# Kernel tuning notes

Measured on AMD Instinct MI355X. Metric: run time of the kernel, lower is better.

The kernel has to match this reference:

```python
import jax, jax.numpy as jnp
import numpy as np

N_NODES = 100000
N_EDGES = 3200000

def setup_inputs() -> dict:
    key = jax.random.key(0)
    ks = jax.random.split(key, 6)
    x = jax.random.normal(ks[0], (N_NODES, 128), dtype=jnp.float32)
    edge_index = jax.random.randint(ks[1], (2, N_EDGES), 0, N_NODES, dtype=jnp.int64)
    W1 = jax.random.normal(ks[2], (128, 64), dtype=jnp.float32) * 0.05
    b1 = jnp.zeros((64,), dtype=jnp.float32)
    W2 = jax.random.normal(ks[3], (64, 64), dtype=jnp.float32) * 0.05
    b2 = jnp.zeros((64,), dtype=jnp.float32)
    Wf = jax.random.normal(ks[4], (64, 40), dtype=jnp.float32) * 0.05
    bf = jnp.zeros((40,), dtype=jnp.float32)
    return {"x": x, "edge_index": edge_index, "W1": W1, "b1": b1,
            "W2": W2, "b2": b2, "Wf": Wf, "bf": bf}

def _gcn_graph(edge_index, n_nodes):
    # Add self loops (PyG GCNConv default), compute symmetric norm.
    loop = jnp.arange(n_nodes, dtype=edge_index.dtype)
    src = jnp.concatenate([edge_index[0], loop])
    dst = jnp.concatenate([edge_index[1], loop])
    deg = jax.ops.segment_sum(jnp.ones_like(dst, dtype=jnp.float32), dst,
                              num_segments=n_nodes)
    dinv = jnp.where(deg > 0, jax.lax.rsqrt(deg), 0.0)
    norm = dinv[src] * dinv[dst]  # [E+N]
    return src, dst, norm

def _gcn_layer(x, W, b, src, dst, norm, n_nodes):
    h = x @ W                     # transform first (as PyG GCNConv)
    msg = h[src] * norm[:, None]  # gather + scale
    agg = jax.ops.segment_sum(msg, dst, num_segments=n_nodes)  # scatter-sum
    return agg + b

def reference(x, edge_index, W1, b1, W2, b2, Wf, bf):
    n = x.shape[0]
    src, dst, norm = _gcn_graph(edge_index, n)
    h = jax.nn.relu(_gcn_layer(x, W1, b1, src, dst, norm, n))
    h = jax.nn.relu(_gcn_layer(h, W2, b2, src, dst, norm, n))
    logits = h @ Wf + bf
    return jax.nn.log_softmax(logits, axis=1)
```

## Files before the change

### kernel.cpp

```cpp
#include <hip/hip_runtime.h>
#include <hip/hip_fp16.h>
#include <cstdint>
#include <cstddef>
#include <cmath>


#define T1  4096
#define CAP 12288

typedef _Float16 half8 __attribute__((ext_vector_type(8)));
typedef float f32x4 __attribute__((ext_vector_type(4)));
typedef float f32x2 __attribute__((ext_vector_type(2)));

__global__ __launch_bounds__(512) void k_init(int* __restrict__ cursor1, int NB) {
    int t = threadIdx.x;
    for (int i = t; i < NB; i += 512) cursor1[i] = i * CAP;
}

__global__ __launch_bounds__(256) void k_pass1(const int* __restrict__ src,
        const int* __restrict__ dst, int* __restrict__ cursor1,
        unsigned int* __restrict__ tmp, int E, int NB) {
    __shared__ unsigned int pack[T1];
    __shared__ unsigned short bkt[T1];
    __shared__ int h[512], hs_[512], gbase[512];
    int t = threadIdx.x;
    for (int i = t; i < 512; i += 256) h[i] = 0;
    __syncthreads();
    int base = blockIdx.x * T1;
    int n = min(T1, E - base);
    unsigned int pk[16];
    int bl[16];
    #pragma unroll
    for (int i = 0; i < 16; ++i) {
        int idx = i * 256 + t;
        if (idx < n) {
            int s_ = src[base + idx], d = dst[base + idx];
            int b = d >> 8;
            pk[i] = (unsigned int)s_ | ((unsigned int)(d & 255) << 17);
            int lo = atomicAdd(&h[b], 1);
            bl[i] = (b << 13) | lo;
        } else bl[i] = -1;
    }
    __syncthreads();
    hs_[t] = h[t]; hs_[t + 256] = h[t + 256];
    __syncthreads();
    for (int st = 1; st < 512; st <<= 1) {
        int v0 = (t >= st) ? hs_[t - st] : 0;
        int v1 = (t + 256 >= st) ? hs_[t + 256 - st] : 0;
        __syncthreads();
        hs_[t] += v0; hs_[t + 256] += v1;
        __syncthreads();
    }
    for (int i = t; i < NB; i += 256)
        gbase[i] = h[i] ? atomicAdd(&cursor1[i], h[i]) : 0;
    __syncthreads();
    #pragma unroll
    for (int i = 0; i < 16; ++i) {
        if (bl[i] >= 0) {
            int b = bl[i] >> 13, lo = bl[i] & 8191;
            int slot = hs_[b] - h[b] + lo;
            pack[slot] = pk[i];
            bkt[slot]  = (unsigned short)b;
        }
    }
    __syncthreads();
    for (int s_ = t; s_ < n; s_ += 256) {
        int b = bkt[s_];
        tmp[gbase[b] + (s_ - (hs_[b] - h[b]))] = pack[s_];
    }
}

__global__ __launch_bounds__(256) void k_p2(const unsigned int* __restrict__ tmp,
        const int* __restrict__ cursor1, int* __restrict__ rowptr,
        int* __restrict__ cnt, int* __restrict__ csrc,
        float* __restrict__ dinv, int N) {
    __shared__ int c[256], cur[256];
    int t = threadIdx.x, b = blockIdx.x;
    c[t] = 0;
    __syncthreads();
    int s0 = b * CAP, s1 = cursor1[b];
    for (int s = s0 + t; s < s1; s += 256)
        atomicAdd(&c[(tmp[s] >> 17) & 255], 1);
    __syncthreads();
    int v = c[t];
    cur[t] = v;
    __syncthreads();
    for (int st = 1; st < 256; st <<= 1) {
        int p = (t >= st) ? cur[t - st] : 0;
        __syncthreads();
        cur[t] += p;
        __syncthreads();
    }
    int rp = s0 + cur[t] - v;
    int node = b * 256 + t;
    if (node < N) {
        rowptr[node] = rp;
        cnt[node]    = v;
        dinv[node]   = rsqrtf((float)v + 1.0f);
    }
    cur[t] = rp;
    __syncthreads();
    for (int s = s0 + t; s < s1; s += 256) {
        unsigned int p = tmp[s];
        int q = atomicAdd(&cur[(p >> 17) & 255], 1);
        csrc[q] = (int)(p & 0x1FFFFu);
    }
}

__global__ __launch_bounds__(256) void k_agg(const int* __restrict__ rowptr,
        const int* __restrict__ cnt, const int* __restrict__ csrc,
        const unsigned int* __restrict__ hp, float* __restrict__ acc, int N) {
    int w = (blockIdx.x * 256 + threadIdx.x) >> 6;
    int lane = threadIdx.x & 63;
    if (w >= N) return;
    int grp = lane >> 4, sub = lane & 15;
    int rs = rowptr[w], re = rs + cnt[w];
    float a0 = 0.f, a1 = 0.f, a2 = 0.f, a3 = 0.f;
    if (grp == 0) {
        unsigned v = hp[((size_t)w << 4) + sub];
        f32x2 lo = __builtin_amdgcn_cvt_pk_f32_fp8((int)v, false);
        f32x2 hi = __builtin_amdgcn_cvt_pk_f32_fp8((int)v, true);
        a0 = lo[0]; a1 = lo[1]; a2 = hi[0]; a3 = hi[1];
    }
    int e = rs + grp;
    for (; e + 12 < re; e += 16) {
        int u0 = csrc[e], u1 = csrc[e + 4], u2 = csrc[e + 8], u3 = csrc[e + 12];
        unsigned v0 = hp[((size_t)u0 << 4) + sub];
        unsigned v1 = hp[((size_t)u1 << 4) + sub];
        unsigned v2 = hp[((size_t)u2 << 4) + sub];
        unsigned v3 = hp[((size_t)u3 << 4) + sub];
        f32x2 l0 = __builtin_amdgcn_cvt_pk_f32_fp8((int)v0, false);
        f32x2 h0 = __builtin_amdgcn_cvt_pk_f32_fp8((int)v0, true);
        f32x2 l1 = __builtin_amdgcn_cvt_pk_f32_fp8((int)v1, false);
        f32x2 h1 = __builtin_amdgcn_cvt_pk_f32_fp8((int)v1, true);
        f32x2 l2 = __builtin_amdgcn_cvt_pk_f32_fp8((int)v2, false);
        f32x2 h2 = __builtin_amdgcn_cvt_pk_f32_fp8((int)v2, true);
        f32x2 l3 = __builtin_amdgcn_cvt_pk_f32_fp8((int)v3, false);
        f32x2 h3 = __builtin_amdgcn_cvt_pk_f32_fp8((int)v3, true);
        a0 += l0[0]; a1 += l0[1]; a2 += h0[0]; a3 += h0[1];
        a0 += l1[0]; a1 += l1[1]; a2 += h1[0]; a3 += h1[1];
        a0 += l2[0]; a1 += l2[1]; a2 += h2[0]; a3 += h2[1];
        a0 += l3[0]; a1 += l3[1]; a2 += h3[0]; a3 += h3[1];
    }
    for (; e < re; e += 4) {
        unsigned v = hp[((size_t)csrc[e] << 4) + sub];
        f32x2 lo = __builtin_amdgcn_cvt_pk_f32_fp8((int)v, false);
        f32x2 hi = __builtin_amdgcn_cvt_pk_f32_fp8((int)v, true);
        a0 += lo[0]; a1 += lo[1]; a2 += hi[0]; a3 += hi[1];
    }
    a0 += __shfl_xor(a0, 16, 64); a0 += __shfl_xor(a0, 32, 64);
    a1 += __shfl_xor(a1, 16, 64); a1 += __shfl_xor(a1, 32, 64);
    a2 += __shfl_xor(a2, 16, 64); a2 += __shfl_xor(a2, 32, 64);
    a3 += __shfl_xor(a3, 16, 64); a3 += __shfl_xor(a3, 32, 64);
    if (grp == 0) {
        float* op = acc + ((size_t)w << 6) + sub;
        op[0]  = a0;
        op[16] = a1;
        op[32] = a2;
        op[48] = a3;
    }
}

__global__ __launch_bounds__(256) void k_xform1(const float* __restrict__ x,
        const float* __restrict__ W1, const float* __restrict__ dinv,
        unsigned int* __restrict__ hs, int N, int ntiles) {
    int t = threadIdx.x;
    int lane = t & 63, wid = t >> 6;
    int r16 = lane & 15, kg = lane >> 4;
    half8 bf[4][4];
    #pragma unroll
    for (int ct = 0; ct < 4; ++ct)
        #pragma unroll
        for (int kt = 0; kt < 4; ++kt) {
            const float* wp = W1 + (kt * 32 + kg * 8) * 64 + ct * 16 + r16;
            half8 h;
            #pragma unroll
            for (int j = 0; j < 8; ++j) h[j] = (_Float16)wp[j * 64];
            bf[ct][kt] = h;
        }
    int wtile = blockIdx.x * 4 + wid;
    int nw = gridDim.x * 4;
    for (int tile = wtile; tile < ntiles; tile += nw) {
        int v0 = tile * 16;
        int rowA = min(v0 + r16, N - 1);
        const float* xp = x + (size_t)rowA * 128 + kg * 8;
        half8 af[4];
        #pragma unroll
        for (int kt = 0; kt < 4; ++kt) {
            float4 p = *(const float4*)(xp + kt * 32);
            float4 q = *(const float4*)(xp + kt * 32 + 4);
            half8 a;
            a[0] = (_Float16)p.x; a[1] = (_Float16)p.y;
            a[2] = (_Float16)p.z; a[3] = (_Float16)p.w;
            a[4] = (_Float16)q.x; a[5] = (_Float16)q.y;
            a[6] = (_Float16)q.z; a[7] = (_Float16)q.w;
            af[kt] = a;
        }
        f32x4 acc0 = {0,0,0,0}, acc1 = {0,0,0,0}, acc2 = {0,0,0,0}, acc3 = {0,0,0,0};
        #pragma unroll
        for (int kt = 0; kt < 4; ++kt) {
            acc0 = __builtin_amdgcn_mfma_f32_16x16x32_f16(af[kt], bf[0][kt], acc0, 0, 0, 0);
            acc1 = __builtin_amdgcn_mfma_f32_16x16x32_f16(af[kt], bf[1][kt], acc1, 0, 0, 0);
            acc2 = __builtin_amdgcn_mfma_f32_16x16x32_f16(af[kt], bf[2][kt], acc2, 0, 0, 0);
            acc3 = __builtin_amdgcn_mfma_f32_16x16x32_f16(af[kt], bf[3][kt], acc3, 0, 0, 0);
        }
        #pragma unroll
        for (int r = 0; r < 4; ++r) {
            int node = v0 + kg * 4 + r;
            if (node < N) {
                float d = dinv[node];
                int pk = __builtin_amdgcn_cvt_pk_fp8_f32(d * acc0[r], d * acc1[r], 0, false);
                pk     = __builtin_amdgcn_cvt_pk_fp8_f32(d * acc2[r], d * acc3[r], pk, true);
                hs[((size_t)node << 4) + r16] = (unsigned int)pk;
            }
        }
    }
}

__global__ __launch_bounds__(256) void k_xform2(const float* __restrict__ acc_in,
        const float* __restrict__ W2, const float* __restrict__ b1,
        const float* __restrict__ dinv, unsigned int* __restrict__ hs2, int N, int ntiles) {
    int t = threadIdx.x;
    int lane = t & 63, wid = t >> 6;
    int r16 = lane & 15, kg = lane >> 4;
    half8 bf[4][2];
    #pragma unroll
    for (int ct = 0; ct < 4; ++ct)
        #pragma unroll
        for (int kt = 0; kt < 2; ++kt) {
            const float* wp = W2 + (kt * 32 + kg * 8) * 64 + ct * 16 + r16;
            half8 h;
            #pragma unroll
            for (int j = 0; j < 8; ++j) h[j] = (_Float16)wp[j * 64];
            bf[ct][kt] = h;
        }
    float b1r[2][8];
    #pragma unroll
    for (int kt = 0; kt < 2; ++kt)
        #pragma unroll
        for (int j = 0; j < 8; ++j) b1r[kt][j] = b1[kt * 32 + kg * 8 + j];
    int wtile = blockIdx.x * 4 + wid;
    int nw = gridDim.x * 4;
    for (int tile = wtile; tile < ntiles; tile += nw) {
        int v0 = tile * 16;
        int rowA = min(v0 + r16, N - 1);
        float da = dinv[rowA];
        const float* ap = acc_in + ((size_t)rowA << 6) + kg * 8;
        half8 af[2];
        #pragma unroll
        for (int kt = 0; kt < 2; ++kt) {
            float4 p = *(const float4*)(ap + kt * 32);
            float4 q = *(const float4*)(ap + kt * 32 + 4);
            half8 a;
            a[0] = (_Float16)fmaxf(fmaf(da, p.x, b1r[kt][0]), 0.f);
            a[1] = (_Float16)fmaxf(fmaf(da, p.y, b1r[kt][1]), 0.f);
            a[2] = (_Float16)fmaxf(fmaf(da, p.z, b1r[kt][2]), 0.f);
            a[3] = (_Float16)fmaxf(fmaf(da, p.w, b1r[kt][3]), 0.f);
            a[4] = (_Float16)fmaxf(fmaf(da, q.x, b1r[kt][4]), 0.f);
            a[5] = (_Float16)fmaxf(fmaf(da, q.y, b1r[kt][5]), 0.f);
            a[6] = (_Float16)fmaxf(fmaf(da, q.z, b1r[kt][6]), 0.f);
            a[7] = (_Float16)fmaxf(fmaf(da, q.w, b1r[kt][7]), 0.f);
            af[kt] = a;
        }
        f32x4 acc0 = {0,0,0,0}, acc1 = {0,0,0,0}, acc2 = {0,0,0,0}, acc3 = {0,0,0,0};
        #pragma unroll
        for (int kt = 0; kt < 2; ++kt) {
            acc0 = __builtin_amdgcn_mfma_f32_16x16x32_f16(af[kt], bf[0][kt], acc0, 0, 0, 0);
            acc1 = __builtin_amdgcn_mfma_f32_16x16x32_f16(af[kt], bf[1][kt], acc1, 0, 0, 0);
            acc2 = __builtin_amdgcn_mfma_f32_16x16x32_f16(af[kt], bf[2][kt], acc2, 0, 0, 0);
            acc3 = __builtin_amdgcn_mfma_f32_16x16x32_f16(af[kt], bf[3][kt], acc3, 0, 0, 0);
        }
        #pragma unroll
        for (int r = 0; r < 4; ++r) {
            int node = v0 + kg * 4 + r;
            if (node < N) {
                float d = dinv[node];
                int pk = __builtin_amdgcn_cvt_pk_fp8_f32(d * acc0[r], d * acc1[r], 0, false);
                pk     = __builtin_amdgcn_cvt_pk_fp8_f32(d * acc2[r], d * acc3[r], pk, true);
                hs2[((size_t)node << 4) + r16] = (unsigned int)pk;
            }
        }
    }
}

__global__ __launch_bounds__(256) void k_final(const float* __restrict__ acc2,
        const float* __restrict__ Wf, const float* __restrict__ b2,
        const float* __restrict__ bf, const float* __restrict__ dinv,
        float* __restrict__ out, int N, int ntiles) {
    int t = threadIdx.x;
    int lane = t & 63, wid = t >> 6;
    int r16 = lane & 15, kg = lane >> 4;
    half8 bfr[3][2];
    #pragma unroll
    for (int ct = 0; ct < 3; ++ct)
        #pragma unroll
        for (int kt = 0; kt < 2; ++kt) {
            int col = ct * 16 + r16;
            half8 h;
            #pragma unroll
            for (int j = 0; j < 8; ++j) {
                int k = kt * 32 + kg * 8 + j;
                h[j] = (col < 40) ? (_Float16)Wf[k * 40 + col] : (_Float16)0.f;
            }
            bfr[ct][kt] = h;
        }
    float b2r[2][8];
    #pragma unroll
    for (int kt = 0; kt < 2; ++kt)
        #pragma unroll
        for (int j = 0; j < 8; ++j) b2r[kt][j] = b2[kt * 32 + kg * 8 + j];
    float bf0 = bf[r16];
    float bf1 = bf[16 + r16];
    float bf2 = (r16 < 8) ? bf[32 + r16] : 0.f;
    int wtile = blockIdx.x * 4 + wid;
    int nw = gridDim.x * 4;
    for (int tile = wtile; tile < ntiles; tile += nw) {
        int v0 = tile * 16;
        int rowA = min(v0 + r16, N - 1);
        float da = dinv[rowA];
        const float* ap = acc2 + ((size_t)rowA << 6) + kg * 8;
        half8 af[2];
        #pragma unroll
        for (int kt = 0; kt < 2; ++kt) {
            float4 p = *(const float4*)(ap + kt * 32);
            float4 q = *(const float4*)(ap + kt * 32 + 4);
            half8 a;
            a[0] = (_Float16)fmaxf(fmaf(da, p.x, b2r[kt][0]), 0.f);
            a[1] = (_Float16)fmaxf(fmaf(da, p.y, b2r[kt][1]), 0.f);
            a[2] = (_Float16)fmaxf(fmaf(da, p.z, b2r[kt][2]), 0.f);
            a[3] = (_Float16)fmaxf(fmaf(da, p.w, b2r[kt][3]), 0.f);
            a[4] = (_Float16)fmaxf(fmaf(da, q.x, b2r[kt][4]), 0.f);
            a[5] = (_Float16)fmaxf(fmaf(da, q.y, b2r[kt][5]), 0.f);
            a[6] = (_Float16)fmaxf(fmaf(da, q.z, b2r[kt][6]), 0.f);
            a[7] = (_Float16)fmaxf(fmaf(da, q.w, b2r[kt][7]), 0.f);
            af[kt] = a;
        }
        f32x4 a0 = {0,0,0,0}, a1 = {0,0,0,0}, a2 = {0,0,0,0};
        #pragma unroll
        for (int kt = 0; kt < 2; ++kt) {
            a0 = __builtin_amdgcn_mfma_f32_16x16x32_f16(af[kt], bfr[0][kt], a0, 0, 0, 0);
            a1 = __builtin_amdgcn_mfma_f32_16x16x32_f16(af[kt], bfr[1][kt], a1, 0, 0, 0);
            a2 = __builtin_amdgcn_mfma_f32_16x16x32_f16(af[kt], bfr[2][kt], a2, 0, 0, 0);
        }
        #pragma unroll
        for (int r = 0; r < 4; ++r) {
            float z0 = a0[r] + bf0;
            float z1 = a1[r] + bf1;
            float z2 = (r16 < 8) ? (a2[r] + bf2) : -INFINITY;
            float m = fmaxf(fmaxf(z0, z1), z2);
            #pragma unroll
            for (int o = 8; o; o >>= 1) m = fmaxf(m, __shfl_xor(m, o, 64));
            float s = expf(z0 - m) + expf(z1 - m) + ((r16 < 8) ? expf(z2 - m) : 0.f);
            #pragma unroll
            for (int o = 8; o; o >>= 1) s += __shfl_xor(s, o, 64);
            float ls = m + logf(s);
            int node = v0 + kg * 4 + r;
            if (node < N) {
                float* op = out + (size_t)node * 40;
                op[r16]      = z0 - ls;
                op[16 + r16] = z1 - ls;
                if (r16 < 8) op[32 + r16] = z2 - ls;
            }
        }
    }
}

extern "C" void kernel_launch(void* const* d_in, const int* in_sizes, int n_in,
                              void* d_out, int out_size, void* d_ws, size_t ws_size,
                              hipStream_t stream) {
    const float* x  = (const float*)d_in[0];
    const int*   ei = (const int*)d_in[1];
    const float* W1 = (const float*)d_in[2];
    const float* b1 = (const float*)d_in[3];
    const float* W2 = (const float*)d_in[4];
    const float* b2 = (const float*)d_in[5];
    const float* Wf = (const float*)d_in[6];
    const float* bf = (const float*)d_in[7];
    float* out = (float*)d_out;

    const int N = in_sizes[0] / 128;
    const int E = in_sizes[1] / 2;
    const int* src = ei;
    const int* dst = ei + E;
    const int NB = (N + 255) >> 8;

    auto align = [](size_t s) { return (s + 255) & ~(size_t)255; };
    char* ws = (char*)d_ws;
    size_t o = 0;
    int*   rowptr  = (int*)(ws + o);   o += align((size_t)N * 4);
    int*   cnt     = (int*)(ws + o);   o += align((size_t)N * 4);
    float* dinv    = (float*)(ws + o); o += align((size_t)N * 4);
    int*   cursor1 = (int*)(ws + o);   o += align(512 * 4);
    int*   csrc    = (int*)(ws + o);   o += align((size_t)NB * CAP * 4);
    unsigned int* B1 = (unsigned int*)(ws + o); o += align((size_t)N * 64);
    float*  B2     = (float*)(ws + o);  o += align((size_t)N * 64 * 4);
    unsigned int* tmp = (unsigned int*)B2;

    int blkT  = (E + T1 - 1) / T1;
    int ntile = (N + 15) / 16;
    int gX = 512;

    k_init <<<1,    512, 0, stream>>>(cursor1, NB);
    k_pass1<<<blkT, 256, 0, stream>>>(src, dst, cursor1, tmp, E, NB);
    k_p2   <<<NB,   256, 0, stream>>>(tmp, cursor1, rowptr, cnt, csrc, dinv, N);

    int blkAgg = (N * 64 + 255) / 256;
    k_xform1<<<gX, 256, 0, stream>>>(x, W1, dinv, B1, N, ntile);
    k_agg   <<<blkAgg, 256, 0, stream>>>(rowptr, cnt, csrc, B1, B2, N);
    k_xform2<<<gX, 256, 0, stream>>>(B2, W2, b1, dinv, B1, N, ntile);
    k_agg   <<<blkAgg, 256, 0, stream>>>(rowptr, cnt, csrc, B1, B2, N);
    k_final <<<gX, 256, 0, stream>>>(B2, Wf, b2, bf, dinv, out, N, ntile);
}
```

Before: 213.2 us.

## Split feature table into two half-width planes and aggregate each in separate passes

The fp8 node feature table is split into two planes of 32 features (8 dwords per node), and each SpMM aggregation runs twice, once per plane, writing to separate fp32 accumulator planes. The transform kernels write and read the split layout. The aim is a smaller gathered working set per pass (about 3.2 MB per plane instead of 6.4 MB) so random gathers hit cache more often. Edge-index loads and accumulator stores are also marked nontemporal. The cost is reading the CSR index array twice per layer and launching two extra kernels.

```diff
diff --git a/kernel.cpp b/kernel.cpp
--- a/kernel.cpp
+++ b/kernel.cpp
@@ -107,28 +107,31 @@
     }
 }
 
-__global__ __launch_bounds__(256) void k_agg(const int* __restrict__ rowptr,
+__global__ __launch_bounds__(256) void k_aggH(const int* __restrict__ rowptr,
         const int* __restrict__ cnt, const int* __restrict__ csrc,
-        const unsigned int* __restrict__ hp, float* __restrict__ acc, int N) {
+        const unsigned int* __restrict__ hp, float* __restrict__ accH, int N) {
     int w = (blockIdx.x * 256 + threadIdx.x) >> 6;
     int lane = threadIdx.x & 63;
     if (w >= N) return;
-    int grp = lane >> 4, sub = lane & 15;
+    int grp = lane >> 3, sub = lane & 7;
     int rs = rowptr[w], re = rs + cnt[w];
     float a0 = 0.f, a1 = 0.f, a2 = 0.f, a3 = 0.f;
     if (grp == 0) {
-        unsigned v = hp[((size_t)w << 4) + sub];
+        unsigned v = hp[((size_t)w << 3) + sub];
         f32x2 lo = __builtin_amdgcn_cvt_pk_f32_fp8((int)v, false);
         f32x2 hi = __builtin_amdgcn_cvt_pk_f32_fp8((int)v, true);
         a0 = lo[0]; a1 = lo[1]; a2 = hi[0]; a3 = hi[1];
     }
     int e = rs + grp;
-    for (; e + 12 < re; e += 16) {
-        int u0 = csrc[e], u1 = csrc[e + 4], u2 = csrc[e + 8], u3 = csrc[e + 12];
-        unsigned v0 = hp[((size_t)u0 << 4) + sub];
-        unsigned v1 = hp[((size_t)u1 << 4) + sub];
-        unsigned v2 = hp[((size_t)u2 << 4) + sub];
-        unsigned v3 = hp[((size_t)u3 << 4) + sub];
+    for (; e + 24 < re; e += 32) {
+        int u0 = __builtin_nontemporal_load(csrc + e);
+        int u1 = __builtin_nontemporal_load(csrc + e + 8);
+        int u2 = __builtin_nontemporal_load(csrc + e + 16);
+        int u3 = __builtin_nontemporal_load(csrc + e + 24);
+        unsigned v0 = hp[((size_t)u0 << 3) + sub];
+        unsigned v1 = hp[((size_t)u1 << 3) + sub];
+        unsigned v2 = hp[((size_t)u2 << 3) + sub];
+        unsigned v3 = hp[((size_t)u3 << 3) + sub];
         f32x2 l0 = __builtin_amdgcn_cvt_pk_f32_fp8((int)v0, false);
         f32x2 h0 = __builtin_amdgcn_cvt_pk_f32_fp8((int)v0, true);
         f32x2 l1 = __builtin_amdgcn_cvt_pk_f32_fp8((int)v1, false);
@@ -142,22 +145,22 @@
         a0 += l2[0]; a1 += l2[1]; a2 += h2[0]; a3 += h2[1];
         a0 += l3[0]; a1 += l3[1]; a2 += h3[0]; a3 += h3[1];
     }
-    for (; e < re; e += 4) {
-        unsigned v = hp[((size_t)csrc[e] << 4) + sub];
+    for (; e < re; e += 8) {
+        unsigned v = hp[((size_t)__builtin_nontemporal_load(csrc + e) << 3) + sub];
         f32x2 lo = __builtin_amdgcn_cvt_pk_f32_fp8((int)v, false);
         f32x2 hi = __builtin_amdgcn_cvt_pk_f32_fp8((int)v, true);
         a0 += lo[0]; a1 += lo[1]; a2 += hi[0]; a3 += hi[1];
     }
-    a0 += __shfl_xor(a0, 16, 64); a0 += __shfl_xor(a0, 32, 64);
-    a1 += __shfl_xor(a1, 16, 64); a1 += __shfl_xor(a1, 32, 64);
-    a2 += __shfl_xor(a2, 16, 64); a2 += __shfl_xor(a2, 32, 64);
-    a3 += __shfl_xor(a3, 16, 64); a3 += __shfl_xor(a3, 32, 64);
+    a0 += __shfl_xor(a0, 8, 64); a0 += __shfl_xor(a0, 16, 64); a0 += __shfl_xor(a0, 32, 64);
+    a1 += __shfl_xor(a1, 8, 64); a1 += __shfl_xor(a1, 16, 64); a1 += __shfl_xor(a1, 32, 64);
+    a2 += __shfl_xor(a2, 8, 64); a2 += __shfl_xor(a2, 16, 64); a2 += __shfl_xor(a2, 32, 64);
+    a3 += __shfl_xor(a3, 8, 64); a3 += __shfl_xor(a3, 16, 64); a3 += __shfl_xor(a3, 32, 64);
     if (grp == 0) {
-        float* op = acc + ((size_t)w << 6) + sub;
-        op[0]  = a0;
-        op[16] = a1;
-        op[32] = a2;
-        op[48] = a3;
+        float* op = accH + ((size_t)w << 5) + sub;
+        __builtin_nontemporal_store(a0, op);
+        __builtin_nontemporal_store(a1, op + 8);
+        __builtin_nontemporal_store(a2, op + 16);
+        __builtin_nontemporal_store(a3, op + 24);
     }
 }
 
@@ -167,6 +170,7 @@
     int t = threadIdx.x;
     int lane = t & 63, wid = t >> 6;
     int r16 = lane & 15, kg = lane >> 4;
+    size_t strideH = (size_t)N * 8;
     half8 bf[4][4];
     #pragma unroll
     for (int ct = 0; ct < 4; ++ct)
@@ -204,6 +208,7 @@
             acc2 = __builtin_amdgcn_mfma_f32_16x16x32_f16(af[kt], bf[2][kt], acc2, 0, 0, 0);
             acc3 = __builtin_amdgcn_mfma_f32_16x16x32_f16(af[kt], bf[3][kt], acc3, 0, 0, 0);
         }
+        unsigned int* hpOut = hs + (size_t)(r16 >> 3) * strideH + (r16 & 7);
         #pragma unroll
         for (int r = 0; r < 4; ++r) {
             int node = v0 + kg * 4 + r;
@@ -211,18 +216,20 @@
                 float d = dinv[node];
                 int pk = __builtin_amdgcn_cvt_pk_fp8_f32(d * acc0[r], d * acc1[r], 0, false);
                 pk     = __builtin_amdgcn_cvt_pk_fp8_f32(d * acc2[r], d * acc3[r], pk, true);
-                hs[((size_t)node << 4) + r16] = (unsigned int)pk;
+                hpOut[(size_t)node << 3] = (unsigned int)pk;
             }
         }
     }
 }
 
-__global__ __launch_bounds__(256) void k_xform2(const float* __restrict__ acc_in,
-        const float* __restrict__ W2, const float* __restrict__ b1,
-        const float* __restrict__ dinv, unsigned int* __restrict__ hs2, int N, int ntiles) {
+__global__ __launch_bounds__(256) void k_xform2(const float* __restrict__ accA,
+        const float* __restrict__ accB, const float* __restrict__ W2,
+        const float* __restrict__ b1, const float* __restrict__ dinv,
+        unsigned int* __restrict__ hs2, int N, int ntiles) {
     int t = threadIdx.x;
     int lane = t & 63, wid = t >> 6;
     int r16 = lane & 15, kg = lane >> 4;
+    size_t strideH = (size_t)N * 8;
     half8 bf[4][2];
     #pragma unroll
     for (int ct = 0; ct < 4; ++ct)
@@ -239,18 +246,20 @@
     for (int kt = 0; kt < 2; ++kt)
         #pragma unroll
         for (int j = 0; j < 8; ++j) b1r[kt][j] = b1[kt * 32 + kg * 8 + j];
+    const float* accSel = (kg & 1) ? accB : accA;
+    int subOff = (kg >> 1) << 3;
     int wtile = blockIdx.x * 4 + wid;
     int nw = gridDim.x * 4;
     for (int tile = wtile; tile < ntiles; tile += nw) {
         int v0 = tile * 16;
         int rowA = min(v0 + r16, N - 1);
         float da = dinv[rowA];
-        const float* ap = acc_in + ((size_t)rowA << 6) + kg * 8;
+        const float* ap = accSel + ((size_t)rowA << 5) + subOff;
         half8 af[2];
         #pragma unroll
         for (int kt = 0; kt < 2; ++kt) {
-            float4 p = *(const float4*)(ap + kt * 32);
-            float4 q = *(const float4*)(ap + kt * 32 + 4);
+            float4 p = *(const float4*)(ap + kt * 16);
+            float4 q = *(const float4*)(ap + kt * 16 + 4);
             half8 a;
             a[0] = (_Float16)fmaxf(fmaf(da, p.x, b1r[kt][0]), 0.f);
             a[1] = (_Float16)fmaxf(fmaf(da, p.y, b1r[kt][1]), 0.f);
@@ -270,6 +279,7 @@
             acc2 = __builtin_amdgcn_mfma_f32_16x16x32_f16(af[kt], bf[2][kt], acc2, 0, 0, 0);
             acc3 = __builtin_amdgcn_mfma_f32_16x16x32_f16(af[kt], bf[3][kt], acc3, 0, 0, 0);
         }
+        unsigned int* hpOut = hs2 + (size_t)(r16 >> 3) * strideH + (r16 & 7);
         #pragma unroll
         for (int r = 0; r < 4; ++r) {
             int node = v0 + kg * 4 + r;
@@ -277,16 +287,16 @@
                 float d = dinv[node];
                 int pk = __builtin_amdgcn_cvt_pk_fp8_f32(d * acc0[r], d * acc1[r], 0, false);
                 pk     = __builtin_amdgcn_cvt_pk_fp8_f32(d * acc2[r], d * acc3[r], pk, true);
-                hs2[((size_t)node << 4) + r16] = (unsigned int)pk;
+                hpOut[(size_t)node << 3] = (unsigned int)pk;
             }
         }
     }
 }
 
-__global__ __launch_bounds__(256) void k_final(const float* __restrict__ acc2,
-        const float* __restrict__ Wf, const float* __restrict__ b2,
-        const float* __restrict__ bf, const float* __restrict__ dinv,
-        float* __restrict__ out, int N, int ntiles) {
+__global__ __launch_bounds__(256) void k_final(const float* __restrict__ accA,
+        const float* __restrict__ accB, const float* __restrict__ Wf,
+        const float* __restrict__ b2, const float* __restrict__ bf,
+        const float* __restrict__ dinv, float* __restrict__ out, int N, int ntiles) {
     int t = threadIdx.x;
     int lane = t & 63, wid = t >> 6;
     int r16 = lane & 15, kg = lane >> 4;
@@ -312,18 +322,20 @@
     float bf0 = bf[r16];
     float bf1 = bf[16 + r16];
     float bf2 = (r16 < 8) ? bf[32 + r16] : 0.f;
+    const float* accSel = (kg & 1) ? accB : accA;
+    int subOff = (kg >> 1) << 3;
     int wtile = blockIdx.x * 4 + wid;
     int nw = gridDim.x * 4;
     for (int tile = wtile; tile < ntiles; tile += nw) {
         int v0 = tile * 16;
         int rowA = min(v0 + r16, N - 1);
         float da = dinv[rowA];
-        const float* ap = acc2 + ((size_t)rowA << 6) + kg * 8;
+        const float* ap = accSel + ((size_t)rowA << 5) + subOff;
         half8 af[2];
         #pragma unroll
         for (int kt = 0; kt < 2; ++kt) {
-            float4 p = *(const float4*)(ap + kt * 32);
-            float4 q = *(const float4*)(ap + kt * 32 + 4);
+            float4 p = *(const float4*)(ap + kt * 16);
+            float4 q = *(const float4*)(ap + kt * 16 + 4);
             half8 a;
             a[0] = (_Float16)fmaxf(fmaf(da, p.x, b2r[kt][0]), 0.f);
             a[1] = (_Float16)fmaxf(fmaf(da, p.y, b2r[kt][1]), 0.f);
@@ -392,9 +404,12 @@
     float* dinv    = (float*)(ws + o); o += align((size_t)N * 4);
     int*   cursor1 = (int*)(ws + o);   o += align(512 * 4);
     int*   csrc    = (int*)(ws + o);   o += align((size_t)NB * CAP * 4);
-    unsigned int* B1 = (unsigned int*)(ws + o); o += align((size_t)N * 64);
-    float*  B2     = (float*)(ws + o);  o += align((size_t)N * 64 * 4);
-    unsigned int* tmp = (unsigned int*)B2;
+    unsigned int* B1 = (unsigned int*)(ws + o); o += align((size_t)N * 16 * 4);
+    float* accA    = (float*)(ws + o); o += align((size_t)N * 32 * 4);
+    float* accB    = (float*)(ws + o); o += align((size_t)N * 32 * 4);
+    unsigned int* tmp = (unsigned int*)accA;
+    unsigned int* hsA = B1;
+    unsigned int* hsB = B1 + (size_t)N * 8;
 
     int blkT  = (E + T1 - 1) / T1;
     int ntile = (N + 15) / 16;
@@ -406,8 +421,10 @@
 
     int blkAgg = (N * 64 + 255) / 256;
     k_xform1<<<gX, 256, 0, stream>>>(x, W1, dinv, B1, N, ntile);
-    k_agg   <<<blkAgg, 256, 0, stream>>>(rowptr, cnt, csrc, B1, B2, N);
-    k_xform2<<<gX, 256, 0, stream>>>(B2, W2, b1, dinv, B1, N, ntile);
-    k_agg   <<<blkAgg, 256, 0, stream>>>(rowptr, cnt, csrc, B1, B2, N);
-    k_final <<<gX, 256, 0, stream>>>(B2, Wf, b2, bf, dinv, out, N, ntile);
-}
+    k_aggH  <<<blkAgg, 256, 0, stream>>>(rowptr, cnt, csrc, hsA, accA, N);
+    k_aggH  <<<blkAgg, 256, 0, stream>>>(rowptr, cnt, csrc, hsB, accB, N);
+    k_xform2<<<gX, 256, 0, stream>>>(accA, accB, W2, b1, dinv, B1, N, ntile);
+    k_aggH  <<<blkAgg, 256, 0, stream>>>(rowptr, cnt, csrc, hsA, accA, N);
+    k_aggH  <<<blkAgg, 256, 0, stream>>>(rowptr, cnt, csrc, hsB, accB, N);
+    k_final <<<gX, 256, 0, stream>>>(accA, accB, Wf, b2, bf, dinv, out, N, ntile);
+}
```

After: 301.2 us. 41.3% more time.

## Fuse first feature transform into CSR build kernel with 128-node buckets

Applied to the files above, without the earlier changes.

Destination buckets shrink from 256 to 128 nodes, with per-bucket capacity halved and the histogram and scan arrays widened to 1024 entries. This gives the CSR second pass twice as many blocks. The first-layer x@W1 MFMA transform, plus its dinv scaling and fp8 packing, is folded into the end of that CSR kernel, so each block transforms its own 128 nodes using dinv held in shared memory. This removes a separate launch and the global dinv re-read. In exchange, the heavier fused kernel carries more registers and serialises the transform behind the CSR scatter within each block.

```diff
diff --git a/kernel.cpp b/kernel.cpp
--- a/kernel.cpp
+++ b/kernel.cpp
@@ -6,7 +6,8 @@
 
 
 #define T1  4096
-#define CAP 12288
+#define BSH 7
+#define CAP 6144
 
 typedef _Float16 half8 __attribute__((ext_vector_type(8)));
 typedef float f32x4 __attribute__((ext_vector_type(4)));
@@ -22,9 +23,9 @@
         unsigned int* __restrict__ tmp, int E, int NB) {
     __shared__ unsigned int pack[T1];
     __shared__ unsigned short bkt[T1];
-    __shared__ int h[512], hs_[512], gbase[512];
+    __shared__ int h[1024], hs_[1024], gbase[1024];
     int t = threadIdx.x;
-    for (int i = t; i < 512; i += 256) h[i] = 0;
+    for (int i = t; i < 1024; i += 256) h[i] = 0;
     __syncthreads();
     int base = blockIdx.x * T1;
     int n = min(T1, E - base);
@@ -35,20 +36,26 @@
         int idx = i * 256 + t;
         if (idx < n) {
             int s_ = src[base + idx], d = dst[base + idx];
-            int b = d >> 8;
-            pk[i] = (unsigned int)s_ | ((unsigned int)(d & 255) << 17);
+            int b = d >> BSH;
+            pk[i] = (unsigned int)s_ | ((unsigned int)(d & 127) << 17);
             int lo = atomicAdd(&h[b], 1);
             bl[i] = (b << 13) | lo;
         } else bl[i] = -1;
     }
     __syncthreads();
-    hs_[t] = h[t]; hs_[t + 256] = h[t + 256];
-    __syncthreads();
-    for (int st = 1; st < 512; st <<= 1) {
-        int v0 = (t >= st) ? hs_[t - st] : 0;
-        int v1 = (t + 256 >= st) ? hs_[t + 256 - st] : 0;
+    #pragma unroll
+    for (int i = 0; i < 4; ++i) hs_[t + i * 256] = h[t + i * 256];
+    __syncthreads();
+    for (int st = 1; st < 1024; st <<= 1) {
+        int tp[4];
+        #pragma unroll
+        for (int i = 0; i < 4; ++i) {
+            int idx = t + i * 256;
+            tp[i] = (idx >= st) ? hs_[idx - st] : 0;
+        }
         __syncthreads();
-        hs_[t] += v0; hs_[t + 256] += v1;
+        #pragma unroll
+        for (int i = 0; i < 4; ++i) hs_[t + i * 256] += tp[i];
         __syncthreads();
     }
     for (int i = t; i < NB; i += 256)
@@ -70,40 +77,97 @@
     }
 }
 
-__global__ __launch_bounds__(256) void k_p2(const unsigned int* __restrict__ tmp,
+__global__ __launch_bounds__(256) void k_p2x(const unsigned int* __restrict__ tmp,
         const int* __restrict__ cursor1, int* __restrict__ rowptr,
-        int* __restrict__ cnt, int* __restrict__ csrc,
-        float* __restrict__ dinv, int N) {
-    __shared__ int c[256], cur[256];
+        int* __restrict__ cnt, int* __restrict__ csrc, float* __restrict__ dinv,
+        const float* __restrict__ x, const float* __restrict__ W1,
+        unsigned int* __restrict__ hs, int N) {
+    __shared__ int c[128], cur[128];
+    __shared__ float sdinv[128];
     int t = threadIdx.x, b = blockIdx.x;
-    c[t] = 0;
+    if (t < 128) c[t] = 0;
     __syncthreads();
     int s0 = b * CAP, s1 = cursor1[b];
     for (int s = s0 + t; s < s1; s += 256)
-        atomicAdd(&c[(tmp[s] >> 17) & 255], 1);
-    __syncthreads();
-    int v = c[t];
-    cur[t] = v;
-    __syncthreads();
-    for (int st = 1; st < 256; st <<= 1) {
-        int p = (t >= st) ? cur[t - st] : 0;
+        atomicAdd(&c[(tmp[s] >> 17) & 127], 1);
+    __syncthreads();
+    int v = 0;
+    if (t < 128) { v = c[t]; cur[t] = v; }
+    __syncthreads();
+    for (int st = 1; st < 128; st <<= 1) {
+        int p = (t < 128 && t >= st) ? cur[t - st] : 0;
         __syncthreads();
-        cur[t] += p;
+        if (t < 128) cur[t] += p;
         __syncthreads();
     }
-    int rp = s0 + cur[t] - v;
-    int node = b * 256 + t;
-    if (node < N) {
-        rowptr[node] = rp;
-        cnt[node]    = v;
-        dinv[node]   = rsqrtf((float)v + 1.0f);
-    }
-    cur[t] = rp;
+    int node = b * 128 + t;
+    if (t < 128) {
+        int rp = s0 + cur[t] - v;
+        float dv = rsqrtf((float)v + 1.0f);
+        sdinv[t] = dv;
+        if (node < N) {
+            rowptr[node] = rp;
+            cnt[node]    = v;
+            dinv[node]   = dv;
+        }
+        cur[t] = rp;
+    }
     __syncthreads();
     for (int s = s0 + t; s < s1; s += 256) {
         unsigned int p = tmp[s];
-        int q = atomicAdd(&cur[(p >> 17) & 255], 1);
+        int q = atomicAdd(&cur[(p >> 17) & 127], 1);
         csrc[q] = (int)(p & 0x1FFFFu);
+    }
+    __syncthreads();
+    int lane = t & 63, wid = t >> 6;
+    int r16 = lane & 15, kg = lane >> 4;
+    half8 bf[4][4];
+    #pragma unroll
+    for (int ct = 0; ct < 4; ++ct)
+        #pragma unroll
+        for (int kt = 0; kt < 4; ++kt) {
+            const float* wp = W1 + (kt * 32 + kg * 8) * 64 + ct * 16 + r16;
+            half8 h;
+            #pragma unroll
+            for (int j = 0; j < 8; ++j) h[j] = (_Float16)wp[j * 64];
+            bf[ct][kt] = h;
+        }
+    #pragma unroll
+    for (int lt2 = 0; lt2 < 2; ++lt2) {
+        int lt = wid * 2 + lt2;
+        int v0 = b * 128 + lt * 16;
+        int rowA = min(v0 + r16, N - 1);
+        const float* xp = x + (size_t)rowA * 128 + kg * 8;
+        half8 af[4];
+        #pragma unroll
+        for (int kt = 0; kt < 4; ++kt) {
+            float4 p = *(const float4*)(xp + kt * 32);
+            float4 q = *(const float4*)(xp + kt * 32 + 4);
+            half8 a;
+            a[0] = (_Float16)p.x; a[1] = (_Float16)p.y;
+            a[2] = (_Float16)p.z; a[3] = (_Float16)p.w;
+            a[4] = (_Float16)q.x; a[5] = (_Float16)q.y;
+            a[6] = (_Float16)q.z; a[7] = (_Float16)q.w;
+            af[kt] = a;
+        }
+        f32x4 acc0 = {0,0,0,0}, acc1 = {0,0,0,0}, acc2 = {0,0,0,0}, acc3 = {0,0,0,0};
+        #pragma unroll
+        for (int kt = 0; kt < 4; ++kt) {
+            acc0 = __builtin_amdgcn_mfma_f32_16x16x32_f16(af[kt], bf[0][kt], acc0, 0, 0, 0);
+            acc1 = __builtin_amdgcn_mfma_f32_16x16x32_f16(af[kt], bf[1][kt], acc1, 0, 0, 0);
+            acc2 = __builtin_amdgcn_mfma_f32_16x16x32_f16(af[kt], bf[2][kt], acc2, 0, 0, 0);
+            acc3 = __builtin_amdgcn_mfma_f32_16x16x32_f16(af[kt], bf[3][kt], acc3, 0, 0, 0);
+        }
+        #pragma unroll
+        for (int r = 0; r < 4; ++r) {
+            int nd = v0 + kg * 4 + r;
+            if (nd < N) {
+                float d = sdinv[lt * 16 + kg * 4 + r];
+                int pk = __builtin_amdgcn_cvt_pk_fp8_f32(d * acc0[r], d * acc1[r], 0, false);
+                pk     = __builtin_amdgcn_cvt_pk_fp8_f32(d * acc2[r], d * acc3[r], pk, true);
+                hs[((size_t)nd << 4) + r16] = (unsigned int)pk;
+            }
+        }
     }
 }
 
@@ -161,62 +225,6 @@
     }
 }
 
-__global__ __launch_bounds__(256) void k_xform1(const float* __restrict__ x,
-        const float* __restrict__ W1, const float* __restrict__ dinv,
-        unsigned int* __restrict__ hs, int N, int ntiles) {
-    int t = threadIdx.x;
-    int lane = t & 63, wid = t >> 6;
-    int r16 = lane & 15, kg = lane >> 4;
-    half8 bf[4][4];
-    #pragma unroll
-    for (int ct = 0; ct < 4; ++ct)
-        #pragma unroll
-        for (int kt = 0; kt < 4; ++kt) {
-            const float* wp = W1 + (kt * 32 + kg * 8) * 64 + ct * 16 + r16;
-            half8 h;
-            #pragma unroll
-            for (int j = 0; j < 8; ++j) h[j] = (_Float16)wp[j * 64];
-            bf[ct][kt] = h;
-        }
-    int wtile = blockIdx.x * 4 + wid;
-    int nw = gridDim.x * 4;
-    for (int tile = wtile; tile < ntiles; tile += nw) {
-        int v0 = tile * 16;
-        int rowA = min(v0 + r16, N - 1);
-        const float* xp = x + (size_t)rowA * 128 + kg * 8;
-        half8 af[4];
-        #pragma unroll
-        for (int kt = 0; kt < 4; ++kt) {
-            float4 p = *(const float4*)(xp + kt * 32);
-            float4 q = *(const float4*)(xp + kt * 32 + 4);
-            half8 a;
-            a[0] = (_Float16)p.x; a[1] = (_Float16)p.y;
-            a[2] = (_Float16)p.z; a[3] = (_Float16)p.w;
-            a[4] = (_Float16)q.x; a[5] = (_Float16)q.y;
-            a[6] = (_Float16)q.z; a[7] = (_Float16)q.w;
-            af[kt] = a;
-        }
-        f32x4 acc0 = {0,0,0,0}, acc1 = {0,0,0,0}, acc2 = {0,0,0,0}, acc3 = {0,0,0,0};
-        #pragma unroll
-        for (int kt = 0; kt < 4; ++kt) {
-            acc0 = __builtin_amdgcn_mfma_f32_16x16x32_f16(af[kt], bf[0][kt], acc0, 0, 0, 0);
-            acc1 = __builtin_amdgcn_mfma_f32_16x16x32_f16(af[kt], bf[1][kt], acc1, 0, 0, 0);
-            acc2 = __builtin_amdgcn_mfma_f32_16x16x32_f16(af[kt], bf[2][kt], acc2, 0, 0, 0);
-            acc3 = __builtin_amdgcn_mfma_f32_16x16x32_f16(af[kt], bf[3][kt], acc3, 0, 0, 0);
-        }
-        #pragma unroll
-        for (int r = 0; r < 4; ++r) {
-            int node = v0 + kg * 4 + r;
-            if (node < N) {
-                float d = dinv[node];
-                int pk = __builtin_amdgcn_cvt_pk_fp8_f32(d * acc0[r], d * acc1[r], 0, false);
-                pk     = __builtin_amdgcn_cvt_pk_fp8_f32(d * acc2[r], d * acc3[r], pk, true);
-                hs[((size_t)node << 4) + r16] = (unsigned int)pk;
-            }
-        }
-    }
-}
-
 __global__ __launch_bounds__(256) void k_xform2(const float* __restrict__ acc_in,
         const float* __restrict__ W2, const float* __restrict__ b1,
         const float* __restrict__ dinv, unsigned int* __restrict__ hs2, int N, int ntiles) {
@@ -382,7 +390,7 @@
     const int E = in_sizes[1] / 2;
     const int* src = ei;
     const int* dst = ei + E;
-    const int NB = (N + 255) >> 8;
+    const int NB = (N + 127) >> BSH;
 
     auto align = [](size_t s) { return (s + 255) & ~(size_t)255; };
     char* ws = (char*)d_ws;
@@ -390,7 +398,7 @@
     int*   rowptr  = (int*)(ws + o);   o += align((size_t)N * 4);
     int*   cnt     = (int*)(ws + o);   o += align((size_t)N * 4);
     float* dinv    = (float*)(ws + o); o += align((size_t)N * 4);
-    int*   cursor1 = (int*)(ws + o);   o += align(512 * 4);
+    int*   cursor1 = (int*)(ws + o);   o += align(1024 * 4);
     int*   csrc    = (int*)(ws + o);   o += align((size_t)NB * CAP * 4);
     unsigned int* B1 = (unsigned int*)(ws + o); o += align((size_t)N * 64);
     float*  B2     = (float*)(ws + o);  o += align((size_t)N * 64 * 4);
@@ -402,10 +410,10 @@
 
     k_init <<<1,    512, 0, stream>>>(cursor1, NB);
     k_pass1<<<blkT, 256, 0, stream>>>(src, dst, cursor1, tmp, E, NB);
-    k_p2   <<<NB,   256, 0, stream>>>(tmp, cursor1, rowptr, cnt, csrc, dinv, N);
+    k_p2x  <<<NB,   256, 0, stream>>>(tmp, cursor1, rowptr, cnt, csrc, dinv,
+                                      x, W1, B1, N);
 
     int blkAgg = (N * 64 + 255) / 256;
-    k_xform1<<<gX, 256, 0, stream>>>(x, W1, dinv, B1, N, ntile);
     k_agg   <<<blkAgg, 256, 0, stream>>>(rowptr, cnt, csrc, B1, B2, N);
     k_xform2<<<gX, 256, 0, stream>>>(B2, W2, b1, dinv, B1, N, ntile);
     k_agg   <<<blkAgg, 256, 0, stream>>>(rowptr, cnt, csrc, B1, B2, N);
```

After: 213.9 us. Within noise of the previous version (+0.3%).
